# Kernel optimization log

Measured on AMD Instinct MI355X. Metric: run time of the kernel, lower is better.

## Reference

```python
import jax, jax.numpy as jnp
import numpy as np

D_IN = 2048
D_OUT = 2048
NUM_HEADS = 32
NUM_KV_GROUPS = 8
HEAD_DIM = D_OUT // NUM_HEADS          # 64
GROUP_SIZE = NUM_HEADS // NUM_KV_GROUPS  # 4
BATCH = 2
SEQ = 2048


def _rope(x, cos, sin):
    # x: [b, h, s, d]; cos/sin: [s, d]
    d = x.shape[-1]
    x1, x2 = x[..., : d // 2], x[..., d // 2:]
    rotated = jnp.concatenate((-x2, x1), axis=-1)
    return x * cos[None, None, :, :] + rotated * sin[None, None, :, :]


def setup_inputs() -> dict:
    key = jax.random.key(0)
    ks = jax.random.split(key, 8)
    x = jax.random.normal(ks[0], (BATCH, SEQ, D_IN), dtype=jnp.float32)
    cos = jax.random.normal(ks[1], (SEQ, HEAD_DIM), dtype=jnp.float32)
    sin = jax.random.normal(ks[2], (SEQ, HEAD_DIM), dtype=jnp.float32)
    # causal mask: True above the diagonal = masked out
    mask = jnp.triu(jnp.ones((SEQ, SEQ), dtype=jnp.bool_), k=1)
    s = 0.02
    Wq = jax.random.normal(ks[3], (D_IN, D_OUT), dtype=jnp.float32) * s
    Wk = jax.random.normal(ks[4], (D_IN, NUM_KV_GROUPS * HEAD_DIM), dtype=jnp.float32) * s
    Wv = jax.random.normal(ks[5], (D_IN, NUM_KV_GROUPS * HEAD_DIM), dtype=jnp.float32) * s
    Wo = jax.random.normal(ks[6], (D_OUT, D_OUT), dtype=jnp.float32) * s
    return {"x": x, "cos": cos, "sin": sin, "mask": mask,
            "Wq": Wq, "Wk": Wk, "Wv": Wv, "Wo": Wo}


def reference(x, cos, sin, mask, Wq, Wk, Wv, Wo):
    b, s, _ = x.shape
    # projections (Linear, no bias): weights stored as [d_in, d_out]
    q = (x @ Wq).reshape(b, s, NUM_HEADS, HEAD_DIM).transpose(0, 2, 1, 3)      # [b,H,s,d]
    k = (x @ Wk).reshape(b, s, NUM_KV_GROUPS, HEAD_DIM).transpose(0, 2, 1, 3)  # [b,G,s,d]
    v = (x @ Wv).reshape(b, s, NUM_KV_GROUPS, HEAD_DIM).transpose(0, 2, 1, 3)  # [b,G,s,d]
    q = _rope(q, cos, sin)
    k = _rope(k, cos, sin)
    # GQA broadcast: repeat each KV group group_size times along head axis
    k = jnp.repeat(k, GROUP_SIZE, axis=1)  # [b,H,s,d]
    v = jnp.repeat(v, GROUP_SIZE, axis=1)  # [b,H,s,d]
    scores = jnp.einsum('bhqd,bhkd->bhqk', q, k)
    scores = jnp.where(mask[None, None, :, :], -jnp.inf, scores)
    # original scales AFTER masking: softmax(scores / sqrt(head_dim)); -inf stays -inf
    attn = jax.nn.softmax(scores * (1.0 / np.sqrt(HEAD_DIM)), axis=-1)
    ctx = jnp.einsum('bhqk,bhkd->bqhd', attn, v).reshape(b, s, D_OUT)
    return ctx @ Wo
```

## Files before the change

### kernel.cpp

```cpp
#include <hip/hip_runtime.h>
#include <hip/hip_fp16.h>

#define SEQ    2048
#define DIN    2048
#define DOUT   2048
#define NH     32
#define NKV    8
#define HD     64
#define BB     2

typedef _Float16 half_t;
typedef __attribute__((ext_vector_type(8))) _Float16 half8;
typedef __attribute__((ext_vector_type(4))) _Float16 half4;
typedef __attribute__((ext_vector_type(2))) __fp16   fp16x2;
typedef __attribute__((ext_vector_type(4))) float    floatx4;

union H8U { half8 h; int u[4]; };
union H2I { fp16x2 h; int i; };

__device__ __forceinline__ void gload16(void* l, const void* g) {
    __builtin_amdgcn_global_load_lds(
        (const __attribute__((address_space(1))) void*)g,
        (__attribute__((address_space(3))) void*)l, 16, 0, 0);
}

__global__ void cast_f2h(const float* __restrict__ in, half_t* __restrict__ out, int n4) {
    int i = blockIdx.x * blockDim.x + threadIdx.x;
    if (i < n4) {
        float4 v = ((const float4*)in)[i];
        half4 h;
        h[0] = (half_t)v.x; h[1] = (half_t)v.y; h[2] = (half_t)v.z; h[3] = (half_t)v.w;
        ((half4*)out)[i] = h;
    }
}

__global__ __launch_bounds__(256) void tcast(const float* __restrict__ in, half_t* __restrict__ out,
                                             int Kd, int Nd) {
    __shared__ float T[32][33];
    int x0 = blockIdx.x * 32, y0 = blockIdx.y * 32;
    int tx = threadIdx.x & 31, ty = threadIdx.x >> 5;
    #pragma unroll
    for (int j = 0; j < 4; j++)
        T[ty + j * 8][tx] = in[(size_t)(y0 + ty + j * 8) * Nd + x0 + tx];
    __syncthreads();
    #pragma unroll
    for (int j = 0; j < 4; j++)
        out[(size_t)(x0 + ty + j * 8) * Kd + y0 + tx] = (half_t)T[tx][ty + j * 8];
}

__global__ __launch_bounds__(256) void gemm_qkv(
    const half_t* __restrict__ A, const half_t* __restrict__ Bt,
    const float* __restrict__ cosb, const float* __restrict__ sinb,
    half_t* __restrict__ Qh, half_t* __restrict__ Kh, half_t* __restrict__ Vt)
{
    __shared__ half_t As[4096];
    __shared__ half_t Bs[4096];
    const int K = DIN, M = BB * SEQ;
    int tid = threadIdx.x, wave = tid >> 6, lane = tid & 63;
    int quad = lane >> 4, l15 = lane & 15;
    int m0 = blockIdx.y * 128, n0 = blockIdx.x * 128;
    int wm = (wave >> 1) * 64, wn = (wave & 1) * 64;
    floatx4 acc[4][4] = {};

    int srow[2], skoff[2], sldso[2];
    #pragma unroll
    for (int is = 0; is < 2; is++) {
        int s = is * 256 + tid;
        int p = s >> 3, sc = s & 7;
        int c = sc ^ (p & 7);
        srow[is]  = 2 * p + (c >> 2);
        skoff[is] = (c & 3) * 8;
        sldso[is] = (is * 256 + wave * 64) * 8;
    }
    for (int k0 = 0; k0 < K; k0 += 32) {
        __syncthreads();
        #pragma unroll
        for (int is = 0; is < 2; is++) {
            gload16(&As[sldso[is]], A  + (size_t)(m0 + srow[is]) * K + k0 + skoff[is]);
            gload16(&Bs[sldso[is]], Bt + (size_t)(n0 + srow[is]) * K + k0 + skoff[is]);
        }
        __syncthreads();
        half8 af[4], bf[4];
        #pragma unroll
        for (int i = 0; i < 4; i++) {
            int r = wm + i * 16 + l15, p = r >> 1;
            int sc = (((r & 1) * 4 + quad) ^ (p & 7));
            af[i] = *(const half8*)&As[p * 64 + sc * 8];
            int rn = wn + i * 16 + l15, pn = rn >> 1;
            int scn = (((rn & 1) * 4 + quad) ^ (pn & 7));
            bf[i] = *(const half8*)&Bs[pn * 64 + scn * 8];
        }
        #pragma unroll
        for (int i = 0; i < 4; i++)
            #pragma unroll
            for (int j = 0; j < 4; j++)
                acc[i][j] = __builtin_amdgcn_mfma_f32_16x16x32_f16(af[i], bf[j], acc[i][j], 0, 0, 0);
    }

    const int headg = (n0 + wn) >> 6;
    const int b = m0 >> 11;
    const int s_base = (m0 & 2047) + wm + quad * 4;

    if (headg < 40) {
        const bool isQ = headg < 32;
        const float sc = isQ ? 0.125f * 1.44269504088896f : 1.0f;
        half_t* outp = isQ ? (Qh + (size_t)(b * NH + headg) * SEQ * 64)
                           : (Kh + (size_t)(b * NKV + (headg - 32)) * SEQ * 64);
        #pragma unroll
        for (int i = 0; i < 4; i++)
            #pragma unroll
            for (int r = 0; r < 4; r++) {
                int s = s_base + i * 16 + r;
                #pragma unroll
                for (int j = 0; j < 2; j++) {
                    int d = j * 16 + l15;
                    float x1 = acc[i][j][r], x2 = acc[i][j + 2][r];
                    float c1 = cosb[s * 64 + d],      s1 = sinb[s * 64 + d];
                    float c2 = cosb[s * 64 + d + 32], s2 = sinb[s * 64 + d + 32];
                    outp[(size_t)s * 64 + d]      = (half_t)((x1 * c1 - x2 * s1) * sc);
                    outp[(size_t)s * 64 + d + 32] = (half_t)((x2 * c2 + x1 * s2) * sc);
                }
            }
    } else {
        half_t* vtp = Vt + (size_t)(b * NKV + (headg - 40)) * 64 * SEQ;
        #pragma unroll
        for (int i = 0; i < 4; i++) {
            int s = s_base + i * 16;
            #pragma unroll
            for (int j = 0; j < 4; j++) {
                int d = j * 16 + l15;
                half4 hv;
                hv[0] = (half_t)acc[i][j][0];
                hv[1] = (half_t)acc[i][j][1];
                hv[2] = (half_t)acc[i][j][2];
                hv[3] = (half_t)acc[i][j][3];
                *(half4*)(vtp + (size_t)d * SEQ + s) = hv;
            }
        }
    }
}

__global__ __launch_bounds__(256) void gemm_tn_f(
    const half_t* __restrict__ A, const half_t* __restrict__ Bt,
    float* __restrict__ C, int M, int N, int K)
{
    __shared__ half_t As[4096];
    __shared__ half_t Bs[4096];
    int tid = threadIdx.x, wave = tid >> 6, lane = tid & 63;
    int quad = lane >> 4, l15 = lane & 15;
    int m0 = blockIdx.y * 128, n0 = blockIdx.x * 128;
    int wm = (wave >> 1) * 64, wn = (wave & 1) * 64;
    floatx4 acc[4][4] = {};
    int srow[2], skoff[2], sldso[2];
    #pragma unroll
    for (int is = 0; is < 2; is++) {
        int s = is * 256 + tid;
        int p = s >> 3, sc = s & 7;
        int c = sc ^ (p & 7);
        srow[is]  = 2 * p + (c >> 2);
        skoff[is] = (c & 3) * 8;
        sldso[is] = (is * 256 + wave * 64) * 8;
    }
    for (int k0 = 0; k0 < K; k0 += 32) {
        __syncthreads();
        #pragma unroll
        for (int is = 0; is < 2; is++) {
            gload16(&As[sldso[is]], A  + (size_t)(m0 + srow[is]) * K + k0 + skoff[is]);
            gload16(&Bs[sldso[is]], Bt + (size_t)(n0 + srow[is]) * K + k0 + skoff[is]);
        }
        __syncthreads();
        half8 af[4], bf[4];
        #pragma unroll
        for (int i = 0; i < 4; i++) {
            int r = wm + i * 16 + l15, p = r >> 1;
            int sc = (((r & 1) * 4 + quad) ^ (p & 7));
            af[i] = *(const half8*)&As[p * 64 + sc * 8];
            int rn = wn + i * 16 + l15, pn = rn >> 1;
            int scn = (((rn & 1) * 4 + quad) ^ (pn & 7));
            bf[i] = *(const half8*)&Bs[pn * 64 + scn * 8];
        }
        #pragma unroll
        for (int i = 0; i < 4; i++)
            #pragma unroll
            for (int j = 0; j < 4; j++)
                acc[i][j] = __builtin_amdgcn_mfma_f32_16x16x32_f16(af[i], bf[j], acc[i][j], 0, 0, 0);
    }
    #pragma unroll
    for (int i = 0; i < 4; i++) {
        int row = m0 + wm + i * 16 + quad * 4;
        #pragma unroll
        for (int j = 0; j < 4; j++) {
            int col = n0 + wn + j * 16 + l15;
            #pragma unroll
            for (int r = 0; r < 4; r++)
                C[(size_t)(row + r) * N + col] = acc[i][j][r];
        }
    }
}

__global__ __launch_bounds__(256, 4) void attn(
    const half_t* __restrict__ Qh, const half_t* __restrict__ Kh,
    const half_t* __restrict__ Vt, half_t* __restrict__ ctx)
{
    __shared__ half_t Ks[2][4096];
    __shared__ half_t Vs[2][4096];

    const int tid = threadIdx.x, wave = tid >> 6, lane = tid & 63;
    const int quad = lane >> 4, l15 = lane & 15;
    const int bid = blockIdx.x;
    const int qt = 15 - (bid >> 6);
    const int b  = (bid >> 5) & 1;
    const int h  = bid & 31;
    const int g  = h >> 2;
    const int q0 = qt * 128;
    const int wm = wave * 32;

    const half_t* kp = Kh + (size_t)(b * NKV + g) * SEQ * 64;
    const half_t* vp = Vt + (size_t)(b * NKV + g) * 64 * SEQ;

    half8 qf[2][2];
    {
        const half_t* qpp = Qh + ((size_t)(b * NH + h) * SEQ + q0 + wm) * 64;
        #pragma unroll
        for (int mf = 0; mf < 2; mf++)
            #pragma unroll
            for (int kc = 0; kc < 2; kc++)
                qf[mf][kc] = *(const half8*)(qpp + (size_t)(mf * 16 + l15) * 64 + kc * 32 + quad * 8);
    }

    int koff[2], voff[2], lo[2];
    #pragma unroll
    for (int is = 0; is < 2; is++) {
        int s = is * 256 + tid;
        int p = s >> 3, c = (s & 7) ^ (p & 7);
        koff[is] = p * 64 + c * 8;
        voff[is] = p * SEQ + c * 8;
        lo[is]   = (is * 256 + wave * 64) * 8;
    }

    float m_i[2], l_i[2];
    m_i[0] = m_i[1] = -__builtin_inff();
    l_i[0] = l_i[1] = 0.f;
    floatx4 o[2][4] = {};

    const int ntiles = 2 * qt + 2;
    #pragma unroll
    for (int is = 0; is < 2; is++) {
        gload16(&Ks[0][lo[is]], kp + koff[is]);
        gload16(&Vs[0][lo[is]], vp + voff[is]);
    }

    const int srcA = l15 + ((quad & 1) ? 32 : 0);
    const int srcB = srcA + 16;
    const bool hiK = (quad >> 1) != 0;

    for (int kt = 0; kt < ntiles; kt++) {
        const int cur = kt & 1;
        const int kb  = kt * 64;
        __syncthreads();
        if (kt + 1 < ntiles) {
            const int kb2 = (kt + 1) * 64;
            #pragma unroll
            for (int is = 0; is < 2; is++) {
                gload16(&Ks[cur ^ 1][lo[is]], kp + (size_t)kb2 * 64 + koff[is]);
                gload16(&Vs[cur ^ 1][lo[is]], vp + kb2 + voff[is]);
            }
        }

        if (kb <= q0 + wm + 31) {
            floatx4 sa[2][4] = {};
            #pragma unroll
            for (int kc = 0; kc < 2; kc++)
                #pragma unroll
                for (int kf = 0; kf < 4; kf++) {
                    int row = kf * 16 + l15;
                    int sc = ((kc * 4 + quad) ^ (row & 7));
                    half8 kfr = *(const half8*)&Ks[cur][row * 64 + sc * 8];
                    sa[0][kf] = __builtin_amdgcn_mfma_f32_16x16x32_f16(kfr, qf[0][kc], sa[0][kf], 0, 0, 0);
                    sa[1][kf] = __builtin_amdgcn_mfma_f32_16x16x32_f16(kfr, qf[1][kc], sa[1][kf], 0, 0, 0);
                }

            if (kb + 63 > q0 + wm) {
                #pragma unroll
                for (int kf = 0; kf < 4; kf++)
                    #pragma unroll
                    for (int r = 0; r < 4; r++) {
                        int key = kb + kf * 16 + quad * 4 + r;
                        if (key > q0 + wm + l15)      sa[0][kf][r] = -__builtin_inff();
                        if (key > q0 + wm + 16 + l15) sa[1][kf][r] = -__builtin_inff();
                    }
            }

            int eh[2][4][2];
            float alpha[2];
            #pragma unroll
            for (int mf = 0; mf < 2; mf++) {
                float mt = sa[mf][0][0];
                #pragma unroll
                for (int kf = 0; kf < 4; kf++)
                    #pragma unroll
                    for (int r = 0; r < 4; r++) mt = fmaxf(mt, sa[mf][kf][r]);
                mt = fmaxf(mt, __shfl_xor(mt, 16));
                mt = fmaxf(mt, __shfl_xor(mt, 32));
                float mn = fmaxf(m_i[mf], mt);
                alpha[mf] = exp2f(m_i[mf] - mn);
                m_i[mf] = mn;
                float rs = 0.f;
                #pragma unroll
                for (int kf = 0; kf < 4; kf++) {
                    float e0 = exp2f(sa[mf][kf][0] - mn);
                    float e1 = exp2f(sa[mf][kf][1] - mn);
                    float e2 = exp2f(sa[mf][kf][2] - mn);
                    float e3 = exp2f(sa[mf][kf][3] - mn);
                    rs += (e0 + e1) + (e2 + e3);
                    H2I p01, p23;
                    p01.h = __builtin_amdgcn_cvt_pkrtz(e0, e1);
                    p23.h = __builtin_amdgcn_cvt_pkrtz(e2, e3);
                    eh[mf][kf][0] = p01.i;
                    eh[mf][kf][1] = p23.i;
                }
                rs += __shfl_xor(rs, 16);
                rs += __shfl_xor(rs, 32);
                l_i[mf] = l_i[mf] * alpha[mf] + rs;
                #pragma unroll
                for (int nf = 0; nf < 4; nf++)
                    #pragma unroll
                    for (int r = 0; r < 4; r++) o[mf][nf][r] *= alpha[mf];
            }

            #pragma unroll
            for (int kc = 0; kc < 2; kc++) {
                H8U pf[2];
                #pragma unroll
                for (int mf = 0; mf < 2; mf++) {
                    int a0 = __shfl(eh[mf][2 * kc][0],     srcA);
                    int a1 = __shfl(eh[mf][2 * kc][1],     srcA);
                    int b0 = __shfl(eh[mf][2 * kc + 1][0], srcA);
                    int b1 = __shfl(eh[mf][2 * kc + 1][1], srcA);
                    int c0 = __shfl(eh[mf][2 * kc][0],     srcB);
                    int c1 = __shfl(eh[mf][2 * kc][1],     srcB);
                    int d0 = __shfl(eh[mf][2 * kc + 1][0], srcB);
                    int d1 = __shfl(eh[mf][2 * kc + 1][1], srcB);
                    pf[mf].u[0] = hiK ? b0 : a0;
                    pf[mf].u[1] = hiK ? b1 : a1;
                    pf[mf].u[2] = hiK ? d0 : c0;
                    pf[mf].u[3] = hiK ? d1 : c1;
                }
                #pragma unroll
                for (int nf = 0; nf < 4; nf++) {
                    int row = nf * 16 + l15;
                    int sc = ((kc * 4 + quad) ^ (row & 7));
                    half8 vf = *(const half8*)&Vs[cur][row * 64 + sc * 8];
                    o[0][nf] = __builtin_amdgcn_mfma_f32_16x16x32_f16(vf, pf[0].h, o[0][nf], 0, 0, 0);
                    o[1][nf] = __builtin_amdgcn_mfma_f32_16x16x32_f16(vf, pf[1].h, o[1][nf], 0, 0, 0);
                }
            }
        }
    }

    #pragma unroll
    for (int mf = 0; mf < 2; mf++) {
        float inv = 1.0f / l_i[mf];
        int s = q0 + wm + mf * 16 + l15;
        half_t* op = ctx + (size_t)(b * SEQ + s) * DOUT + h * 64 + quad * 4;
        #pragma unroll
        for (int nf = 0; nf < 4; nf++) {
            half4 hv;
            hv[0] = (half_t)(o[mf][nf][0] * inv);
            hv[1] = (half_t)(o[mf][nf][1] * inv);
            hv[2] = (half_t)(o[mf][nf][2] * inv);
            hv[3] = (half_t)(o[mf][nf][3] * inv);
            *(half4*)(op + nf * 16) = hv;
        }
    }
}

extern "C" void kernel_launch(void* const* d_in, const int* in_sizes, int n_in,
                              void* d_out, int out_size, void* d_ws, size_t ws_size,
                              hipStream_t stream) {
    const float* x    = (const float*)d_in[0];
    const float* cosb = (const float*)d_in[1];
    const float* sinb = (const float*)d_in[2];
    const float* Wq   = (const float*)d_in[4];
    const float* Wk   = (const float*)d_in[5];
    const float* Wv   = (const float*)d_in[6];
    const float* Wo   = (const float*)d_in[7];
    float* out = (float*)d_out;

    const size_t M  = (size_t)BB * SEQ;
    const size_t nX = M * DIN;

    char* ws = (char*)d_ws;
    const size_t MB = 1048576;
    half_t* xh     = (half_t*)(ws);
    half_t* WqkvT  = (half_t*)(ws + 16 * MB);
    half_t* WoT    = (half_t*)(ws + 28 * MB);
    half_t* Qh     = (half_t*)(ws + 36 * MB);
    half_t* Kh     = (half_t*)(ws + 52 * MB);
    half_t* Vt     = (half_t*)(ws + 56 * MB);
    half_t* ctxh   = (half_t*)(ws + 60 * MB);

    cast_f2h<<<(nX / 4) / 256, 256, 0, stream>>>(x, xh, nX / 4);
    tcast<<<dim3(64, 64), 256, 0, stream>>>(Wq, WqkvT, DIN, DOUT);
    tcast<<<dim3(16, 64), 256, 0, stream>>>(Wk, WqkvT + (size_t)2048 * 2048, DIN, 512);
    tcast<<<dim3(16, 64), 256, 0, stream>>>(Wv, WqkvT + (size_t)2560 * 2048, DIN, 512);
    tcast<<<dim3(64, 64), 256, 0, stream>>>(Wo, WoT, DOUT, DOUT);

    gemm_qkv<<<dim3(3072 / 128, M / 128), 256, 0, stream>>>(xh, WqkvT, cosb, sinb, Qh, Kh, Vt);

    attn<<<BB * NH * (SEQ / 128), 256, 0, stream>>>(Qh, Kh, Vt, ctxh);

    gemm_tn_f<<<dim3(DOUT / 128, M / 128), 256, 0, stream>>>(ctxh, WoT, out, M, DOUT, DIN);
}
```

Baseline: 370.3 us.

## Move Q RoPE into attention, balance causal tile order, use hardware exp2

```diff
diff --git a/kernel.cpp b/kernel.cpp
--- a/kernel.cpp
+++ b/kernel.cpp
@@ -18,6 +18,12 @@
 union H8U { half8 h; int u[4]; };
 union H2I { fp16x2 h; int i; };
 
+#if __has_builtin(__builtin_amdgcn_exp2f)
+#define EXP2F(x) __builtin_amdgcn_exp2f(x)
+#else
+#define EXP2F(x) __expf((x) * 0.6931471805599453f)
+#endif
+
 __device__ __forceinline__ void gload16(void* l, const void* g) {
     __builtin_amdgcn_global_load_lds(
         (const __attribute__((address_space(1))) void*)g,
@@ -55,7 +61,7 @@
 {
     __shared__ half_t As[4096];
     __shared__ half_t Bs[4096];
-    const int K = DIN, M = BB * SEQ;
+    const int K = DIN;
     int tid = threadIdx.x, wave = tid >> 6, lane = tid & 63;
     int quad = lane >> 4, l15 = lane & 15;
     int m0 = blockIdx.y * 128, n0 = blockIdx.x * 128;
@@ -101,11 +107,19 @@
     const int b = m0 >> 11;
     const int s_base = (m0 & 2047) + wm + quad * 4;
 
-    if (headg < 40) {
-        const bool isQ = headg < 32;
-        const float sc = isQ ? 0.125f * 1.44269504088896f : 1.0f;
-        half_t* outp = isQ ? (Qh + (size_t)(b * NH + headg) * SEQ * 64)
-                           : (Kh + (size_t)(b * NKV + (headg - 32)) * SEQ * 64);
+    if (headg < 32) {
+        half_t* outp = Qh + (size_t)(b * NH + headg) * SEQ * 64;
+        #pragma unroll
+        for (int i = 0; i < 4; i++)
+            #pragma unroll
+            for (int j = 0; j < 4; j++) {
+                int d = j * 16 + l15;
+                #pragma unroll
+                for (int r = 0; r < 4; r++)
+                    outp[(size_t)(s_base + i * 16 + r) * 64 + d] = (half_t)acc[i][j][r];
+            }
+    } else if (headg < 40) {
+        half_t* outp = Kh + (size_t)(b * NKV + (headg - 32)) * SEQ * 64;
         #pragma unroll
         for (int i = 0; i < 4; i++)
             #pragma unroll
@@ -117,8 +131,8 @@
                     float x1 = acc[i][j][r], x2 = acc[i][j + 2][r];
                     float c1 = cosb[s * 64 + d],      s1 = sinb[s * 64 + d];
                     float c2 = cosb[s * 64 + d + 32], s2 = sinb[s * 64 + d + 32];
-                    outp[(size_t)s * 64 + d]      = (half_t)((x1 * c1 - x2 * s1) * sc);
-                    outp[(size_t)s * 64 + d + 32] = (half_t)((x2 * c2 + x1 * s2) * sc);
+                    outp[(size_t)s * 64 + d]      = (half_t)(x1 * c1 - x2 * s1);
+                    outp[(size_t)s * 64 + d + 32] = (half_t)(x2 * c2 + x1 * s2);
                 }
             }
     } else {
@@ -200,7 +214,8 @@
 
 __global__ __launch_bounds__(256, 4) void attn(
     const half_t* __restrict__ Qh, const half_t* __restrict__ Kh,
-    const half_t* __restrict__ Vt, half_t* __restrict__ ctx)
+    const half_t* __restrict__ Vt, const float* __restrict__ cosb,
+    const float* __restrict__ sinb, half_t* __restrict__ ctx)
 {
     __shared__ half_t Ks[2][4096];
     __shared__ half_t Vs[2][4096];
@@ -208,9 +223,14 @@
     const int tid = threadIdx.x, wave = tid >> 6, lane = tid & 63;
     const int quad = lane >> 4, l15 = lane & 15;
     const int bid = blockIdx.x;
-    const int qt = 15 - (bid >> 6);
-    const int b  = (bid >> 5) & 1;
-    const int h  = bid & 31;
+    const int k  = bid >> 8;
+    const int u  = bid & 255;
+    const int q2 = u & 3;
+    const int bh = u >> 2;
+    const int qt = (k == 0) ? 15 - 2 * q2 : (k == 1) ? 2 * q2
+                 : (k == 2) ? 14 - 2 * q2 : 2 * q2 + 1;
+    const int b  = bh >> 5;
+    const int h  = bh & 31;
     const int g  = h >> 2;
     const int q0 = qt * 128;
     const int wm = wave * 32;
@@ -220,12 +240,32 @@
 
     half8 qf[2][2];
     {
+        const float sc = 0.125f * 1.44269504088896f;
         const half_t* qpp = Qh + ((size_t)(b * NH + h) * SEQ + q0 + wm) * 64;
         #pragma unroll
-        for (int mf = 0; mf < 2; mf++)
-            #pragma unroll
-            for (int kc = 0; kc < 2; kc++)
-                qf[mf][kc] = *(const half8*)(qpp + (size_t)(mf * 16 + l15) * 64 + kc * 32 + quad * 8);
+        for (int mf = 0; mf < 2; mf++) {
+            int s = q0 + wm + mf * 16 + l15;
+            const float* cp = cosb + s * 64 + quad * 8;
+            const float* sp = sinb + s * 64 + quad * 8;
+            half8 xa = *(const half8*)(qpp + (size_t)(mf * 16 + l15) * 64 + quad * 8);
+            half8 xb = *(const half8*)(qpp + (size_t)(mf * 16 + l15) * 64 + 32 + quad * 8);
+            float4 c1a = *(const float4*)(cp),      c1b = *(const float4*)(cp + 4);
+            float4 s1a = *(const float4*)(sp),      s1b = *(const float4*)(sp + 4);
+            float4 c2a = *(const float4*)(cp + 32), c2b = *(const float4*)(cp + 36);
+            float4 s2a = *(const float4*)(sp + 32), s2b = *(const float4*)(sp + 36);
+            const float* c1 = (const float*)&c1a;
+            #pragma unroll
+            for (int t = 0; t < 8; t++) {
+                float cc1 = (t < 4) ? ((const float*)&c1a)[t] : ((const float*)&c1b)[t - 4];
+                float ss1 = (t < 4) ? ((const float*)&s1a)[t] : ((const float*)&s1b)[t - 4];
+                float cc2 = (t < 4) ? ((const float*)&c2a)[t] : ((const float*)&c2b)[t - 4];
+                float ss2 = (t < 4) ? ((const float*)&s2a)[t] : ((const float*)&s2b)[t - 4];
+                float x1 = (float)xa[t], x2 = (float)xb[t];
+                qf[mf][0][t] = (half_t)((x1 * cc1 - x2 * ss1) * sc);
+                qf[mf][1][t] = (half_t)((x2 * cc2 + x1 * ss2) * sc);
+            }
+            (void)c1;
+        }
     }
 
     int koff[2], voff[2], lo[2];
@@ -303,15 +343,15 @@
                 mt = fmaxf(mt, __shfl_xor(mt, 16));
                 mt = fmaxf(mt, __shfl_xor(mt, 32));
                 float mn = fmaxf(m_i[mf], mt);
-                alpha[mf] = exp2f(m_i[mf] - mn);
+                alpha[mf] = EXP2F(m_i[mf] - mn);
                 m_i[mf] = mn;
                 float rs = 0.f;
                 #pragma unroll
                 for (int kf = 0; kf < 4; kf++) {
-                    float e0 = exp2f(sa[mf][kf][0] - mn);
-                    float e1 = exp2f(sa[mf][kf][1] - mn);
-                    float e2 = exp2f(sa[mf][kf][2] - mn);
-                    float e3 = exp2f(sa[mf][kf][3] - mn);
+                    float e0 = EXP2F(sa[mf][kf][0] - mn);
+                    float e1 = EXP2F(sa[mf][kf][1] - mn);
+                    float e2 = EXP2F(sa[mf][kf][2] - mn);
+                    float e3 = EXP2F(sa[mf][kf][3] - mn);
                     rs += (e0 + e1) + (e2 + e3);
                     H2I p01, p23;
                     p01.h = __builtin_amdgcn_cvt_pkrtz(e0, e1);
@@ -408,7 +448,7 @@
 
     gemm_qkv<<<dim3(3072 / 128, M / 128), 256, 0, stream>>>(xh, WqkvT, cosb, sinb, Qh, Kh, Vt);
 
-    attn<<<BB * NH * (SEQ / 128), 256, 0, stream>>>(Qh, Kh, Vt, ctxh);
+    attn<<<BB * NH * (SEQ / 128), 256, 0, stream>>>(Qh, Kh, Vt, cosb, sinb, ctxh);
 
     gemm_tn_f<<<dim3(DOUT / 128, M / 128), 256, 0, stream>>>(ctxh, WoT, out, M, DOUT, DIN);
 }
```

Measured after the change: 359.4 us. 2.9% less time.
